# Optimization experiments

Hardware: AMD Instinct MI355X
Metric: run time of the kernel (lower is better)

The kernel has to match this reference:

```python
import jax, jax.numpy as jnp
import numpy as np

C = 128      # hidden_dim
H = 8        # nheads
HD = C // H  # head_dim = 16
SCALE = HD ** (-0.5)
Q = 100      # num_queries
T = 5        # t
DM = 512     # d_model
AD = 128     # audio feature dim
EPS = 1e-5


def _ln(x, g, b):
    m = jnp.mean(x, -1, keepdims=True)
    v = jnp.mean((x - m) ** 2, -1, keepdims=True)
    return (x - m) / jnp.sqrt(v + EPS) * g + b


def _heads(x):
    bt, L, c = x.shape
    return x.reshape(bt, L, H, c // H).transpose(0, 2, 1, 3)  # (bt,H,L,hd)


def _unheads(x):
    bt, h, L, d = x.shape
    return x.transpose(0, 2, 1, 3).reshape(bt, L, h * d)


def _attn(q, k, v):
    a = jax.nn.softmax(jnp.einsum('bhqd,bhkd->bhqk', q, k) * SCALE, axis=-1)
    return jnp.einsum('bhqk,bhkd->bhqd', a, v)


def setup_inputs() -> dict:
    key = jax.random.key(0)
    ks = iter(jax.random.split(key, 40))
    def nrm(shape, s=0.02):
        return jax.random.normal(next(ks), shape, dtype=jnp.float32) * s
    bt, hw = 40, 1024
    return {
        'audio_feat': jax.random.normal(next(ks), (bt, hw, AD), dtype=jnp.float32),
        'vis_feat': jax.random.normal(next(ks), (bt, hw, DM), dtype=jnp.float32),
        'iq_emb': nrm((Q, C), 0.1),
        'w_iqp': nrm((C, 2 * C)), 'b_iqp': jnp.zeros((2 * C,), jnp.float32),
        'w_afp': nrm((AD, 2 * C)), 'b_afp': jnp.zeros((2 * C,), jnp.float32),
        'w_vfp': nrm((DM, 2 * C)), 'b_vfp': jnp.zeros((2 * C,), jnp.float32),
        'g_an': jnp.ones((2 * C,), jnp.float32), 'be_an': jnp.zeros((2 * C,), jnp.float32),
        'g_vn': jnp.ones((2 * C,), jnp.float32), 'be_vn': jnp.zeros((2 * C,), jnp.float32),
        'w_aqp': nrm((C, 2 * C)), 'b_aqp': jnp.zeros((2 * C,), jnp.float32),
        'w_vqp': nrm((C, 2 * C)), 'b_vqp': jnp.zeros((2 * C,), jnp.float32),
        'w_aq': nrm((AD, C)), 'b_aq': jnp.zeros((C,), jnp.float32),
        'w_vq': nrm((DM, C)), 'b_vq': jnp.zeros((C,), jnp.float32),
        'w_in': nrm((C, 3 * C)), 'b_in': jnp.zeros((3 * C,), jnp.float32),
        'w_o': nrm((C, C)), 'b_o': jnp.zeros((C,), jnp.float32),
        'w_ao': nrm((C, DM)), 'b_ao': jnp.zeros((DM,), jnp.float32),
        'w_vo': nrm((C, DM)), 'b_vo': jnp.zeros((DM,), jnp.float32),
    }


def reference(audio_feat, vis_feat, iq_emb, w_iqp, b_iqp, w_afp, b_afp,
              w_vfp, b_vfp, g_an, be_an, g_vn, be_vn, w_aqp, b_aqp,
              w_vqp, b_vqp, w_aq, b_aq, w_vq, b_vq, w_in, b_in, w_o, b_o,
              w_ao, b_ao, w_vo, b_vo):
    bt, hw, _ = vis_feat.shape
    bs = bt // T

    # intermediate query projection -> audio / vis query sets
    aq0, vq0 = jnp.split(iq_emb @ w_iqp + b_iqp, 2, axis=-1)  # (Q, C) each
    aqh = _heads(jnp.broadcast_to(aq0, (bt, Q, C)))
    vqh = _heads(jnp.broadcast_to(vq0, (bt, Q, C)))

    # feature K/V (LayerNorm over 2C then chunk)
    a_ki, a_vi = jnp.split(_ln(audio_feat @ w_afp + b_afp, g_an, be_an), 2, axis=-1)
    v_ki, v_vi = jnp.split(_ln(vis_feat @ w_vfp + b_vfp, g_vn, be_vn), 2, axis=-1)

    # cross-attn: queries attend to features, with residual on queries
    aiq = _unheads(_attn(aqh, _heads(a_ki), _heads(a_vi)) + aqh)  # (bt,Q,C)
    viq = _unheads(_attn(vqh, _heads(v_ki), _heads(v_vi)) + vqh)

    # self-attn over concatenated queries across time (per sample)
    queries = jnp.concatenate([aiq, viq], axis=1).reshape(bs, T * 2 * Q, C)
    qkv = queries @ w_in + b_in
    q, k, v = jnp.split(qkv, 3, axis=-1)
    sa = _unheads(_attn(_heads(q), _heads(k), _heads(v))) @ w_o + b_o
    queries = sa.reshape(bt, 2 * Q, C)
    aiq2, viq2 = queries[:, :Q], queries[:, Q:]

    # fused queries become K/V for the features
    a_kf, a_vf = jnp.split(aiq2 @ w_aqp + b_aqp, 2, axis=-1)
    v_kf, v_vf = jnp.split(viq2 @ w_vqp + b_vqp, 2, axis=-1)
    _a = _heads(audio_feat @ w_aq + b_aq)
    _v = _heads(vis_feat @ w_vq + b_vq)

    a_att = _unheads(_attn(_a, _heads(v_kf), _heads(v_vf)))  # (bt,hw,C)
    audio_out = (a_att + audio_feat) @ w_ao + b_ao            # (bt,hw,DM)

    v_att = _unheads(_attn(_v, _heads(a_kf), _heads(a_vf)))   # (bt,hw,C)
    vis_out = v_att @ w_vo + b_vo + vis_feat                  # (bt,hw,DM)

    return (audio_out, vis_out, aiq2)
```

## Files before the change

kernel.cpp:

```cpp
#include <hip/hip_runtime.h>

#define EPSF 1e-5f
#define SCALEF 0.25f

typedef __attribute__((ext_vector_type(8))) __bf16 bf16x8;
typedef __attribute__((ext_vector_type(8))) unsigned short sh8;
typedef __attribute__((ext_vector_type(4))) float f32x4;

__device__ __forceinline__ unsigned short f2bf(float f) {
  unsigned u = __float_as_uint(f);
  return (unsigned short)((u + 0x7FFFu + ((u >> 16) & 1u)) >> 16);
}
__device__ __forceinline__ unsigned pk2(float lo, float hi) {
  return (unsigned)f2bf(lo) | ((unsigned)f2bf(hi) << 16);
}
__device__ __forceinline__ float bf2f(unsigned short u) {
  return __uint_as_float((unsigned)u << 16);
}

__device__ __forceinline__ void gll16(const void* g, void* l) {
  __builtin_amdgcn_global_load_lds((const __attribute__((address_space(1))) void*)g,
                                   (__attribute__((address_space(3))) void*)l,
                                   16, 0, 0);
}

template <int K, int BN, int EPI, bool POST, bool AHEAD, bool OBF, bool PBF>
__global__ __launch_bounds__(BN * 2) void mfma_gemm(
    const unsigned short* __restrict__ A, const unsigned short* __restrict__ Wt,
    const float* __restrict__ bias, const float* __restrict__ gg,
    const float* __restrict__ be, const float* __restrict__ post,
    float* __restrict__ C, int M, int Ntot, int ATPB, int CTPB, size_t CPS,
    float* __restrict__ aiq2) {
  constexpr int NW = BN / 32;
  constexpr int NCW = BN / 64;
  __shared__ __align__(16) unsigned short As[128 * 32];
  __shared__ __align__(16) unsigned short Bs[BN * 32];
  __shared__ float2 part[128][4];
  const int tid = threadIdx.x;
  const int wid = tid >> 6, lane = tid & 63;
  const int wr = wid / NCW, wc = wid % NCW;
  const int m0t = blockIdx.x * 128, n0t = blockIdx.y * BN;
  const int ir = lane >> 2, sl = lane & 3;
  const int sg = lane >> 4, li = lane & 15;
  f32x4 acc[4][4];
#pragma unroll
  for (int i = 0; i < 4; i++)
#pragma unroll
    for (int j = 0; j < 4; j++) acc[i][j] = (f32x4){0.f, 0.f, 0.f, 0.f};
  constexpr int nIss = 8 + BN / 16;

  for (int k0 = 0; k0 < K; k0 += 32) {
    __syncthreads();
    for (int is = wid; is < nIss; is += NW) {
      if (is < 8) {
        int r = is * 16 + ir;
        int sp = sl ^ ((r >> 1) & 3);
        const unsigned short* gsrc;
        if (AHEAD) {
          int rg = m0t + r;
          if (rg >= M) rg = M - 1;
          int b = rg / ATPB, tok = rg - b * ATPB;
          int e = k0 + sp * 8;
          gsrc = A + ((((size_t)b * 8 + (e >> 4)) * ATPB + tok) << 4) + (e & 15);
        } else {
          gsrc = A + (size_t)(m0t + r) * K + k0 + sp * 8;
        }
        gll16(gsrc, (void*)&As[is * 512]);
      } else {
        int r = (is - 8) * 16 + ir;
        int sp = sl ^ ((r >> 1) & 3);
        gll16(Wt + (size_t)(n0t + r) * K + k0 + sp * 8, (void*)&Bs[(is - 8) * 512]);
      }
    }
    __syncthreads();
    bf16x8 af[4], bfr[4];
#pragma unroll
    for (int mi = 0; mi < 4; mi++) {
      int m = wr * 64 + mi * 16 + li;
      sh8 t = *(const sh8*)&As[m * 32 + ((sg ^ ((m >> 1) & 3)) << 3)];
      af[mi] = __builtin_bit_cast(bf16x8, t);
    }
#pragma unroll
    for (int ni = 0; ni < 4; ni++) {
      int n = wc * 64 + ni * 16 + li;
      sh8 t = *(const sh8*)&Bs[n * 32 + ((sg ^ ((n >> 1) & 3)) << 3)];
      bfr[ni] = __builtin_bit_cast(bf16x8, t);
    }
#pragma unroll
    for (int mi = 0; mi < 4; mi++)
#pragma unroll
      for (int ni = 0; ni < 4; ni++)
        acc[mi][ni] = __builtin_amdgcn_mfma_f32_16x16x32_bf16(af[mi], bfr[ni],
                                                              acc[mi][ni], 0, 0, 0);
  }

  float bv[4];
#pragma unroll
  for (int ni = 0; ni < 4; ni++) bv[ni] = bias[n0t + wc * 64 + ni * 16 + li];

  if constexpr (EPI == 1) {
#pragma unroll
    for (int mi = 0; mi < 4; mi++)
#pragma unroll
      for (int ni = 0; ni < 4; ni++)
#pragma unroll
        for (int r = 0; r < 4; r++) acc[mi][ni][r] += bv[ni];
#pragma unroll
    for (int mi = 0; mi < 4; mi++)
#pragma unroll
      for (int r = 0; r < 4; r++) {
        float s = acc[mi][0][r] + acc[mi][1][r] + acc[mi][2][r] + acc[mi][3][r];
        float q2 = acc[mi][0][r] * acc[mi][0][r] + acc[mi][1][r] * acc[mi][1][r] +
                   acc[mi][2][r] * acc[mi][2][r] + acc[mi][3][r] * acc[mi][3][r];
#pragma unroll
        for (int off = 1; off < 16; off <<= 1) {
          s += __shfl_xor(s, off);
          q2 += __shfl_xor(q2, off);
        }
        if (li == 0) part[wr * 64 + mi * 16 + sg * 4 + r][wc] = make_float2(s, q2);
      }
    __syncthreads();
    float gv[4], bev[4];
#pragma unroll
    for (int ni = 0; ni < 4; ni++) {
      int col = wc * 64 + ni * 16 + li;
      gv[ni] = gg[col];
      bev[ni] = be[col];
    }
#pragma unroll
    for (int mi = 0; mi < 4; mi++)
#pragma unroll
      for (int r = 0; r < 4; r++) {
        int mrow = wr * 64 + mi * 16 + sg * 4 + r;
        float2 p0 = part[mrow][0], p1 = part[mrow][1], p2 = part[mrow][2], p3 = part[mrow][3];
        float S = p0.x + p1.x + p2.x + p3.x;
        float Qq = p0.y + p1.y + p2.y + p3.y;
        float mean = S * (1.f / 256.f);
        float var = Qq * (1.f / 256.f) - mean * mean;
        float rstd = rsqrtf(var + EPSF);
        int mg = m0t + mrow;
        int b = mg / CTPB, tok = mg - b * CTPB;
#pragma unroll
        for (int ni = 0; ni < 4; ni++) {
          int col = wc * 64 + ni * 16 + li;
          float val = (acc[mi][ni][r] - mean) * rstd * gv[ni] + bev[ni];
          int half = col >> 7, h = (col >> 4) & 7, d = col & 15;
          size_t idx = ((((size_t)b * 8 + h) * CTPB + tok) << 4) + d;
          if (OBF) {
            unsigned short* dst = (unsigned short*)C + (half ? CPS : 0);
            dst[idx] = f2bf(val);
          } else {
            float* dst = half ? (C + CPS) : C;
            dst[idx] = val;
          }
        }
      }
  } else if constexpr (EPI == 2) {
#pragma unroll
    for (int mi = 0; mi < 4; mi++)
#pragma unroll
      for (int r = 0; r < 4; r++) {
        int mg = m0t + wr * 64 + mi * 16 + sg * 4 + r;
        if (mg < M) {
          int b = mg / CTPB, tok = mg - b * CTPB;
#pragma unroll
          for (int ni = 0; ni < 4; ni++) {
            int col = n0t + wc * 64 + ni * 16 + li;
            float v = acc[mi][ni][r] + bv[ni];
            int pt = col >> 7, h = (col >> 4) & 7, d = col & 15;
            size_t idx = ((((size_t)b * 8 + h) * CTPB + tok) << 4) + d;
            if (OBF)
              ((unsigned short*)C + (size_t)pt * CPS)[idx] = f2bf(v);
            else
              (C + (size_t)pt * CPS)[idx] = v;
          }
        }
      }
  } else {
#pragma unroll
    for (int mi = 0; mi < 4; mi++)
#pragma unroll
      for (int r = 0; r < 4; r++) {
        int mrow = m0t + wr * 64 + mi * 16 + sg * 4 + r;
        if (mrow < M) {
#pragma unroll
          for (int ni = 0; ni < 4; ni++) {
            int col = n0t + wc * 64 + ni * 16 + li;
            float v = acc[mi][ni][r] + bv[ni];
            if (POST) {
              if (PBF)
                v += bf2f(((const unsigned short*)post)[(size_t)mrow * Ntot + col]);
              else
                v += post[(size_t)mrow * Ntot + col];
            }
            C[(size_t)mrow * Ntot + col] = v;
            if (aiq2) {
              int fb = mrow / 200, wi2 = mrow % 200;
              if (wi2 < 100) aiq2[((size_t)fb * 100 + wi2) * Ntot + col] = v;
            }
          }
        }
      }
  }
}

__global__ __launch_bounds__(512) void mattn1(
    const float* __restrict__ aqvq,
    const unsigned short* __restrict__ akn, const unsigned short* __restrict__ avn,
    const unsigned short* __restrict__ vkn, const unsigned short* __restrict__ vvn,
    unsigned short* __restrict__ op) {
  __shared__ __align__(16) unsigned short Klds[64][24];
  __shared__ __align__(16) unsigned short VTlds[16][72];
  __shared__ __align__(16) unsigned short Plds[8][16][72];
  const int tid = threadIdx.x, wid = tid >> 6, lane = tid & 63;
  const int li = lane & 15, gr = lane >> 4;
  const int z = blockIdx.z, h = blockIdx.y;
  const int mod = z >= 40 ? 1 : 0;
  const int b = z - mod * 40;
  const int bh = b * 8 + h;
  const int qi = wid * 16 + li;
  const bool qact = qi < 100;
  const int qic = qact ? qi : 99;
  const float* qrow = aqvq + mod * 128 + (size_t)qic * 256 + h * 16;
  const unsigned short* kp = mod ? vkn : akn;
  const unsigned short* vp = mod ? vvn : avn;

  sh8 z8 = (sh8)0;
  bf16x8 qf = __builtin_bit_cast(bf16x8, z8);
  if (gr < 2) {
    const float4* q4 = (const float4*)(qrow + gr * 8);
    float4 qa = q4[0], qb = q4[1];
    sh8 tt;
    tt[0] = f2bf(qa.x); tt[1] = f2bf(qa.y); tt[2] = f2bf(qa.z); tt[3] = f2bf(qa.w);
    tt[4] = f2bf(qb.x); tt[5] = f2bf(qb.y); tt[6] = f2bf(qb.z); tt[7] = f2bf(qb.w);
    qf = __builtin_bit_cast(bf16x8, tt);
  }

  float mrun = -3e38f, lrun = 0.f;
  f32x4 acc = (f32x4){0.f, 0.f, 0.f, 0.f};
  const f32x4 zero4 = (f32x4){0.f, 0.f, 0.f, 0.f};
  const unsigned* Ku = (const unsigned*)(kp + (size_t)bh * 1024 * 16);
  const unsigned* Vu = (const unsigned*)(vp + (size_t)bh * 1024 * 16);
  const int skey = tid >> 3, sdb = tid & 7;

  for (int kb = 0; kb < 1024; kb += 64) {
    __syncthreads();
    unsigned kw = Ku[(size_t)(kb + skey) * 8 + sdb];
    unsigned vw = Vu[(size_t)(kb + skey) * 8 + sdb];
    *(unsigned*)&Klds[skey][sdb * 2] = kw;
    VTlds[sdb * 2 + 0][skey] = (unsigned short)(kw, vw & 0xffff);
    VTlds[sdb * 2 + 1][skey] = (unsigned short)(vw >> 16);
    __syncthreads();
    f32x4 st[4];
#pragma unroll
    for (int t = 0; t < 4; t++) {
      sh8 kk = *(const sh8*)&Klds[t * 16 + li][(gr & 1) * 8];
      st[t] = __builtin_amdgcn_mfma_f32_16x16x32_bf16(
          __builtin_bit_cast(bf16x8, kk), qf, zero4, 0, 0, 0);
    }
    float sv[4][4];
#pragma unroll
    for (int t = 0; t < 4; t++)
#pragma unroll
      for (int r = 0; r < 4; r++) sv[t][r] = st[t][r] * SCALEF;
    float bm = sv[0][0];
#pragma unroll
    for (int t = 0; t < 4; t++)
#pragma unroll
      for (int r = 0; r < 4; r++) bm = fmaxf(bm, sv[t][r]);
    bm = fmaxf(bm, __shfl_xor(bm, 16));
    bm = fmaxf(bm, __shfl_xor(bm, 32));
    float mnew = fmaxf(mrun, bm);
    float cf = __expf(mrun - mnew);
    mrun = mnew;
    lrun *= cf;
    acc[0] *= cf; acc[1] *= cf; acc[2] *= cf; acc[3] *= cf;
    float ls = 0.f;
    unsigned pw[4][2];
#pragma unroll
    for (int t = 0; t < 4; t++) {
      float p0 = __expf(sv[t][0] - mnew), p1 = __expf(sv[t][1] - mnew);
      float p2 = __expf(sv[t][2] - mnew), p3 = __expf(sv[t][3] - mnew);
      ls += (p0 + p1) + (p2 + p3);
      pw[t][0] = pk2(p0, p1);
      pw[t][1] = pk2(p2, p3);
    }
    ls += __shfl_xor(ls, 16);
    ls += __shfl_xor(ls, 32);
    lrun += ls;
#pragma unroll
    for (int t = 0; t < 4; t++)
      *(uint2*)&Plds[wid][li][t * 16 + gr * 4] = make_uint2(pw[t][0], pw[t][1]);
#pragma unroll
    for (int hh = 0; hh < 2; hh++) {
      sh8 vt = *(const sh8*)&VTlds[li][hh * 32 + gr * 8];
      sh8 pt = *(const sh8*)&Plds[wid][li][hh * 32 + gr * 8];
      acc = __builtin_amdgcn_mfma_f32_16x16x32_bf16(
          __builtin_bit_cast(bf16x8, vt), __builtin_bit_cast(bf16x8, pt), acc, 0, 0, 0);
    }
  }
  float inv = 1.f / lrun;
  float o[4];
#pragma unroll
  for (int r = 0; r < 4; r++) o[r] = acc[r] * inv;
  const float4* q4 = (const float4*)(qrow + gr * 4);
  float4 qv = q4[0];
  o[0] += qv.x; o[1] += qv.y; o[2] += qv.z; o[3] += qv.w;
  if (qact) {
    int obh = (b / 5) * 8 + h;
    int otok = (b % 5) * 200 + mod * 100 + qi;
    *(uint2*)(op + (((size_t)obh * 1000 + otok) << 4) + gr * 4) =
        make_uint2(pk2(o[0], o[1]), pk2(o[2], o[3]));
  }
}

template <int MODE>
__global__ __launch_bounds__(512) void mattn8(
    const unsigned short* __restrict__ q0s, const unsigned short* __restrict__ q1s,
    size_t qsb, size_t qsh, int qsr,
    const unsigned short* __restrict__ k0s, const unsigned short* __restrict__ v0s,
    const unsigned short* __restrict__ k1s, const unsigned short* __restrict__ v1s,
    int nk, int nq, unsigned short* __restrict__ o0s, unsigned short* __restrict__ o1s,
    int OTPB, const unsigned short* __restrict__ residbf) {
  __shared__ __align__(16) unsigned short Klds[64][24];
  __shared__ __align__(16) unsigned short VTlds[16][72];
  __shared__ __align__(16) unsigned short Plds[8][16][72];
  const int tid = threadIdx.x, wid = tid >> 6, lane = tid & 63;
  const int li = lane & 15, gr = lane >> 4;
  const int z = blockIdx.z, h = blockIdx.y;
  int mod = 0, b = z;
  const unsigned short *qp = q0s, *kp = k0s, *vp = v0s;
  unsigned short* op = o0s;
  if (MODE == 2) {
    mod = z >= 40 ? 1 : 0;
    b = z - mod * 40;
    if (mod) { qp = q1s; kp = k1s; vp = v1s; op = o1s; }
  }
  const int bh = b * 8 + h;
  const int qi = blockIdx.x * 128 + wid * 16 + li;
  const bool qact = qi < nq;
  const int qic = qact ? qi : nq - 1;
  const unsigned short* qrow = qp + b * qsb + h * qsh + (size_t)qic * qsr;

  sh8 z8 = (sh8)0;
  bf16x8 qf = __builtin_bit_cast(bf16x8, z8);
  if (gr < 2) qf = __builtin_bit_cast(bf16x8, *(const sh8*)(qrow + gr * 8));

  float mrun = -3e38f, lrun = 0.f;
  f32x4 acc = (f32x4){0.f, 0.f, 0.f, 0.f};
  const f32x4 zero4 = (f32x4){0.f, 0.f, 0.f, 0.f};
  const unsigned* Ku = (const unsigned*)(kp + (size_t)bh * nk * 16);
  const unsigned* Vu = (const unsigned*)(vp + (size_t)bh * nk * 16);
  const int skey = tid >> 3, sdb = tid & 7;

  for (int kb = 0; kb < nk; kb += 64) {
    __syncthreads();
    int gk = kb + skey;
    bool ok = gk < nk;
    unsigned kw = ok ? Ku[(size_t)gk * 8 + sdb] : 0u;
    unsigned vw = ok ? Vu[(size_t)gk * 8 + sdb] : 0u;
    *(unsigned*)&Klds[skey][sdb * 2] = kw;
    VTlds[sdb * 2 + 0][skey] = (unsigned short)(vw & 0xffff);
    VTlds[sdb * 2 + 1][skey] = (unsigned short)(vw >> 16);
    __syncthreads();
    f32x4 st[4];
#pragma unroll
    for (int t = 0; t < 4; t++) {
      sh8 kk = *(const sh8*)&Klds[t * 16 + li][(gr & 1) * 8];
      st[t] = __builtin_amdgcn_mfma_f32_16x16x32_bf16(
          __builtin_bit_cast(bf16x8, kk), qf, zero4, 0, 0, 0);
    }
    float sv[4][4];
#pragma unroll
    for (int t = 0; t < 4; t++)
#pragma unroll
      for (int r = 0; r < 4; r++) sv[t][r] = st[t][r] * SCALEF;
    if (kb + 64 > nk) {
#pragma unroll
      for (int t = 0; t < 4; t++) {
        int kbase = kb + t * 16 + gr * 4;
#pragma unroll
        for (int r = 0; r < 4; r++)
          if (kbase + r >= nk) sv[t][r] = -1e30f;
      }
    }
    float bm = sv[0][0];
#pragma unroll
    for (int t = 0; t < 4; t++)
#pragma unroll
      for (int r = 0; r < 4; r++) bm = fmaxf(bm, sv[t][r]);
    bm = fmaxf(bm, __shfl_xor(bm, 16));
    bm = fmaxf(bm, __shfl_xor(bm, 32));
    float mnew = fmaxf(mrun, bm);
    float cf = __expf(mrun - mnew);
    mrun = mnew;
    lrun *= cf;
    acc[0] *= cf; acc[1] *= cf; acc[2] *= cf; acc[3] *= cf;
    float ls = 0.f;
    unsigned pw[4][2];
#pragma unroll
    for (int t = 0; t < 4; t++) {
      float p0 = __expf(sv[t][0] - mnew), p1 = __expf(sv[t][1] - mnew);
      float p2 = __expf(sv[t][2] - mnew), p3 = __expf(sv[t][3] - mnew);
      ls += (p0 + p1) + (p2 + p3);
      pw[t][0] = pk2(p0, p1);
      pw[t][1] = pk2(p2, p3);
    }
    ls += __shfl_xor(ls, 16);
    ls += __shfl_xor(ls, 32);
    lrun += ls;
#pragma unroll
    for (int t = 0; t < 4; t++)
      *(uint2*)&Plds[wid][li][t * 16 + gr * 4] = make_uint2(pw[t][0], pw[t][1]);
#pragma unroll
    for (int hh = 0; hh < 2; hh++) {
      sh8 vt = *(const sh8*)&VTlds[li][hh * 32 + gr * 8];
      sh8 pt = *(const sh8*)&Plds[wid][li][hh * 32 + gr * 8];
      acc = __builtin_amdgcn_mfma_f32_16x16x32_bf16(
          __builtin_bit_cast(bf16x8, vt), __builtin_bit_cast(bf16x8, pt), acc, 0, 0, 0);
    }
  }
  float inv = 1.f / lrun;
  float o[4];
#pragma unroll
  for (int r = 0; r < 4; r++) o[r] = acc[r] * inv;
  if (MODE == 2 && mod == 0 && residbf) {
    uint2 rv = *(const uint2*)(residbf + ((size_t)b * 1024 + qic) * 128 + h * 16 + gr * 4);
    o[0] += bf2f((unsigned short)(rv.x & 0xffff));
    o[1] += bf2f((unsigned short)(rv.x >> 16));
    o[2] += bf2f((unsigned short)(rv.y & 0xffff));
    o[3] += bf2f((unsigned short)(rv.y >> 16));
  }
  if (qact) {
    *(uint2*)(op + (((size_t)bh * OTPB + qi) << 4) + gr * 4) =
        make_uint2(pk2(o[0], o[1]), pk2(o[2], o[3]));
  }
}

__global__ __launch_bounds__(256) void prep_kernel(
    const float* __restrict__ audio, const float* __restrict__ vis,
    const float* __restrict__ iq, const float* __restrict__ w_iqp,
    const float* __restrict__ b_iqp,
    const float* __restrict__ w_afp, const float* __restrict__ w_vfp,
    const float* __restrict__ w_aq, const float* __restrict__ w_vq,
    const float* __restrict__ w_in, const float* __restrict__ w_o,
    const float* __restrict__ w_ao, const float* __restrict__ w_vo,
    unsigned short* __restrict__ WT, unsigned short* __restrict__ audio_bf,
    unsigned short* __restrict__ vis_bf, float* __restrict__ aqvq) {
  __shared__ float row[128];
  const int g = blockIdx.x, tid = threadIdx.x;
  if (g < 12800) {
    const float* in = (g < 2560) ? audio : vis;
    unsigned short* outp = (g < 2560) ? audio_bf : vis_bf;
    int i = (g < 2560 ? g : g - 2560) * 256 + tid;
    float4 a = ((const float4*)in)[i * 2];
    float4 b = ((const float4*)in)[i * 2 + 1];
    uint4 o;
    o.x = pk2(a.x, a.y);
    o.y = pk2(a.z, a.w);
    o.z = pk2(b.x, b.y);
    o.w = pk2(b.z, b.w);
    ((uint4*)outp)[i] = o;
  } else if (g < 14528) {
    int lg = g - 12800;
    int K, N;
    const float* W;
    unsigned dst;
    if (lg < 128)       { K = 128; N = 256; W = w_afp; dst = 0; }
    else if (lg < 640)  { K = 512; N = 256; W = w_vfp; dst = 32768;  lg -= 128; }
    else if (lg < 704)  { K = 128; N = 128; W = w_aq;  dst = 163840; lg -= 640; }
    else if (lg < 960)  { K = 512; N = 128; W = w_vq;  dst = 180224; lg -= 704; }
    else if (lg < 1152) { K = 128; N = 384; W = w_in;  dst = 245760; lg -= 960; }
    else if (lg < 1216) { K = 128; N = 128; W = w_o;   dst = 294912; lg -= 1152; }
    else if (lg < 1472) { K = 128; N = 512; W = w_ao;  dst = 311296; lg -= 1216; }
    else                { K = 128; N = 512; W = w_vo;  dst = 376832; lg -= 1472; }
    int idx = lg * 256 + tid;
    if (idx < K * N) {
      int k = idx / N, n = idx - k * N;
      WT[dst + (size_t)n * K + k] = f2bf(W[idx]);
    }
  } else {
    int r = g - 14528;
    if (tid < 128) row[tid] = iq[r * 128 + tid];
    __syncthreads();
    float acc = b_iqp[tid];
#pragma unroll 8
    for (int k = 0; k < 128; ++k) acc += row[k] * w_iqp[k * 256 + tid];
    aqvq[r * 256 + tid] = acc;
  }
}

template <int K, int N, int R>
__global__ __launch_bounds__(N) void gemm_kv_kernel(
    const float* __restrict__ in,
    const float* __restrict__ Wa, const float* __restrict__ ba,
    const float* __restrict__ Wv, const float* __restrict__ bvv,
    unsigned short* __restrict__ Ka, unsigned short* __restrict__ Va,
    unsigned short* __restrict__ Kv, unsigned short* __restrict__ Vv) {
  __shared__ float rows[R][K];
  const int sel = blockIdx.y;
  const float* W = sel ? Wv : Wa;
  const float* bias = sel ? bvv : ba;
  unsigned short* outK = sel ? Kv : Ka;
  unsigned short* outV = sel ? Vv : Va;
  const int rowoff = sel ? 100 : 0;
  int r0 = blockIdx.x * R;
  for (int e = threadIdx.x; e < R * K; e += N) {
    int rr = e / K, k = e - rr * K;
    size_t r = r0 + rr;
    size_t irx = (r / 100) * 200 + rowoff + (r % 100);
    rows[rr][k] = in[irx * K + k];
  }
  __syncthreads();
  int c = threadIdx.x;
  float acc[R];
  float bb = bias[c];
#pragma unroll
  for (int rr = 0; rr < R; rr++) acc[rr] = bb;
  for (int k = 0; k < K; k += 4) {
    float w0 = W[(size_t)k * N + c];
    float w1 = W[(size_t)(k + 1) * N + c];
    float w2 = W[(size_t)(k + 2) * N + c];
    float w3 = W[(size_t)(k + 3) * N + c];
#pragma unroll
    for (int rr = 0; rr < R; rr++) {
      float4 r4 = *reinterpret_cast<const float4*>(&rows[rr][k]);
      acc[rr] = fmaf(r4.x, w0, acc[rr]);
      acc[rr] = fmaf(r4.y, w1, acc[rr]);
      acc[rr] = fmaf(r4.z, w2, acc[rr]);
      acc[rr] = fmaf(r4.w, w3, acc[rr]);
    }
  }
  int half = c >> 7, h = (c >> 4) & 7, d = c & 15;
  unsigned short* dst = half ? outV : outK;
#pragma unroll
  for (int rr = 0; rr < R; rr++) {
    int r = r0 + rr;
    int b = r / 100, tok = r - b * 100;
    dst[((((size_t)b * 8 + h) * 100 + tok) << 4) + d] = f2bf(acc[rr]);
  }
}

extern "C" void kernel_launch(void* const* d_in, const int* in_sizes, int n_in,
                              void* d_out, int out_size, void* d_ws, size_t ws_size,
                              hipStream_t stream) {
  const float* audio = (const float*)d_in[0];
  const float* vis   = (const float*)d_in[1];
  const float* iq    = (const float*)d_in[2];
  const float* w_iqp = (const float*)d_in[3];
  const float* b_iqp = (const float*)d_in[4];
  const float* w_afp = (const float*)d_in[5];
  const float* b_afp = (const float*)d_in[6];
  const float* w_vfp = (const float*)d_in[7];
  const float* b_vfp = (const float*)d_in[8];
  const float* g_an  = (const float*)d_in[9];
  const float* be_an = (const float*)d_in[10];
  const float* g_vn  = (const float*)d_in[11];
  const float* be_vn = (const float*)d_in[12];
  const float* w_aqp = (const float*)d_in[13];
  const float* b_aqp = (const float*)d_in[14];
  const float* w_vqp = (const float*)d_in[15];
  const float* b_vqp = (const float*)d_in[16];
  const float* w_aq  = (const float*)d_in[17];
  const float* b_aq  = (const float*)d_in[18];
  const float* w_vq  = (const float*)d_in[19];
  const float* b_vq  = (const float*)d_in[20];
  const float* w_in  = (const float*)d_in[21];
  const float* b_in  = (const float*)d_in[22];
  const float* w_o   = (const float*)d_in[23];
  const float* b_o   = (const float*)d_in[24];
  const float* w_ao  = (const float*)d_in[25];
  const float* b_ao  = (const float*)d_in[26];
  const float* w_vo  = (const float*)d_in[27];
  const float* b_vo  = (const float*)d_in[28];

  float* out = (float*)d_out;
  float* ws  = (float*)d_ws;

  unsigned short* vis_bf = (unsigned short*)(out);
  unsigned short* akn = (unsigned short*)(out + 10485760);
  unsigned short* avn = akn + 5242880;
  unsigned short* vkn = akn + 10485760;
  unsigned short* vvn = akn + 15728640;
  unsigned short* a_hm = (unsigned short*)(out + 20971520);
  unsigned short* v_hm = (unsigned short*)(out + 23592960);
  float* aiq2_out = out + 41943040;
  float* audio_out = out;
  float* vis_out   = out + 20971520;

  unsigned short* WT       = (unsigned short*)(ws);
  unsigned short* audio_bf = (unsigned short*)(ws + 262144);
  unsigned short* Q1hm     = (unsigned short*)(ws + 2883584);
  unsigned short* saphm    = (unsigned short*)(ws + 3395584);
  unsigned short* qkvhm    = (unsigned short*)(ws + 3915776);
  unsigned short* aatthm   = (unsigned short*)(ws + 3915776);
  unsigned short* vatthm   = (unsigned short*)(ws + 6987776);
  float* SA                = ws + 9609216;
  unsigned short* Ka = (unsigned short*)(ws + 10633216);
  unsigned short* Va = Ka + 512000;
  unsigned short* Kv = Ka + 1024000;
  unsigned short* Vv = Ka + 1536000;
  float* aqvq = ws + 12681216;

  unsigned short* ao_t = WT + 311296;
  unsigned short* vo_t = WT + 376832;
  unsigned short* afp_t = WT + 0;
  unsigned short* vfp_t = WT + 32768;
  unsigned short* aq_t  = WT + 163840;
  unsigned short* vq_t  = WT + 180224;
  unsigned short* in_t  = WT + 245760;
  unsigned short* o_t   = WT + 294912;

  prep_kernel<<<14628, 256, 0, stream>>>(
      audio, vis, iq, w_iqp, b_iqp, w_afp, w_vfp, w_aq, w_vq, w_in, w_o, w_ao,
      w_vo, WT, audio_bf, vis_bf, aqvq);

  mfma_gemm<128, 256, 1, false, false, true, false><<<dim3(320, 1), 512, 0, stream>>>(
      audio_bf, afp_t, b_afp, g_an, be_an, nullptr, (float*)akn, 40960, 256, 0, 1024,
      5242880, nullptr);
  mfma_gemm<512, 256, 1, false, false, true, false><<<dim3(320, 1), 512, 0, stream>>>(
      vis_bf, vfp_t, b_vfp, g_vn, be_vn, nullptr, (float*)vkn, 40960, 256, 0, 1024,
      5242880, nullptr);

  mattn1<<<dim3(1, 8, 80), 512, 0, stream>>>(aqvq, akn, avn, vkn, vvn, Q1hm);

  mfma_gemm<128, 128, 2, false, true, true, false><<<dim3(63, 3), 256, 0, stream>>>(
      Q1hm, in_t, b_in, nullptr, nullptr, nullptr, (float*)qkvhm, 8000, 384, 1000, 1000,
      1024000, nullptr);

  mattn8<1><<<dim3(8, 8, 8), 512, 0, stream>>>(
      qkvhm, nullptr, 128000, 16000, 16, qkvhm + 1024000, qkvhm + 2048000,
      nullptr, nullptr, 1000, 1000, saphm, nullptr, 1000, nullptr);

  mfma_gemm<128, 128, 0, false, true, false, false><<<dim3(63, 1), 256, 0, stream>>>(
      saphm, o_t, b_o, nullptr, nullptr, nullptr, SA, 8000, 128, 1000, 0, 0, aiq2_out);

  gemm_kv_kernel<128, 256, 16><<<dim3(250, 2), 256, 0, stream>>>(
      SA, w_aqp, b_aqp, w_vqp, b_vqp, Ka, Va, Kv, Vv);

  mfma_gemm<128, 128, 2, false, false, true, false><<<dim3(320, 1), 256, 0, stream>>>(
      audio_bf, aq_t, b_aq, nullptr, nullptr, nullptr, (float*)a_hm, 40960, 128, 0, 1024,
      0, nullptr);
  mfma_gemm<512, 128, 2, false, false, true, false><<<dim3(320, 1), 256, 0, stream>>>(
      vis_bf, vq_t, b_vq, nullptr, nullptr, nullptr, (float*)v_hm, 40960, 128, 0, 1024,
      0, nullptr);

  mattn8<2><<<dim3(8, 8, 80), 512, 0, stream>>>(
      a_hm, v_hm, 131072, 16384, 16, Kv, Vv, Ka, Va, 100, 1024,
      aatthm, vatthm, 1024, audio_bf);

  mfma_gemm<128, 128, 0, true, true, false, true><<<dim3(320, 4), 256, 0, stream>>>(
      vatthm, vo_t, b_vo, nullptr, nullptr, (const float*)vis_bf, vis_out, 40960, 512,
      1024, 0, 0, nullptr);

  mfma_gemm<128, 128, 0, false, true, false, false><<<dim3(320, 4), 256, 0, stream>>>(
      aatthm, ao_t, b_ao, nullptr, nullptr, nullptr, audio_out, 40960, 512, 1024, 0, 0,
      nullptr);
}
```

Before: 348.4 us.

## Fuse fp32-to-bf16 input conversion into first projection GEMMs and prefetch attention K/V

The standalone pass that converted audio and visual features to bf16 is removed. The first projection GEMMs now read fp32 directly, convert to bf16 in registers, and store the tile into LDS and into a side bf16 buffer that later kernels reuse. The attention kernels also register-prefetch the next K/V block before the barrier so the global loads overlap compute. In exchange, the A loads in those GEMMs no longer go through async global-to-LDS and are issued synchronously by threads. Each converted chunk is written only once because the output dimension fits in one block column.

```diff
diff --git a/kernel.cpp b/kernel.cpp
--- a/kernel.cpp
+++ b/kernel.cpp
@@ -24,13 +24,14 @@
                                    16, 0, 0);
 }
 
-template <int K, int BN, int EPI, bool POST, bool AHEAD, bool OBF, bool PBF>
+template <int K, int BN, int EPI, bool POST, bool AHEAD, bool OBF, bool PBF, bool AF32>
 __global__ __launch_bounds__(BN * 2) void mfma_gemm(
     const unsigned short* __restrict__ A, const unsigned short* __restrict__ Wt,
     const float* __restrict__ bias, const float* __restrict__ gg,
     const float* __restrict__ be, const float* __restrict__ post,
     float* __restrict__ C, int M, int Ntot, int ATPB, int CTPB, size_t CPS,
-    float* __restrict__ aiq2) {
+    float* __restrict__ aiq2, const float* __restrict__ Af32,
+    unsigned short* __restrict__ Aside) {
   constexpr int NW = BN / 32;
   constexpr int NCW = BN / 64;
   __shared__ __align__(16) unsigned short As[128 * 32];
@@ -51,25 +52,42 @@
 
   for (int k0 = 0; k0 < K; k0 += 32) {
     __syncthreads();
-    for (int is = wid; is < nIss; is += NW) {
-      if (is < 8) {
-        int r = is * 16 + ir;
-        int sp = sl ^ ((r >> 1) & 3);
-        const unsigned short* gsrc;
-        if (AHEAD) {
-          int rg = m0t + r;
-          if (rg >= M) rg = M - 1;
-          int b = rg / ATPB, tok = rg - b * ATPB;
-          int e = k0 + sp * 8;
-          gsrc = A + ((((size_t)b * 8 + (e >> 4)) * ATPB + tok) << 4) + (e & 15);
+    if constexpr (AF32) {
+      int r = tid >> 2, slp = tid & 3;
+      int sp = slp ^ ((r >> 1) & 3);
+      const float4* src = (const float4*)(Af32 + (size_t)(m0t + r) * K + k0 + sp * 8);
+      float4 aa = src[0], bb = src[1];
+      uint4 w;
+      w.x = pk2(aa.x, aa.y); w.y = pk2(aa.z, aa.w);
+      w.z = pk2(bb.x, bb.y); w.w = pk2(bb.z, bb.w);
+      *(uint4*)&As[r * 32 + slp * 8] = w;
+      *(uint4*)(Aside + (size_t)(m0t + r) * K + k0 + sp * 8) = w;
+      for (int is = 8 + wid; is < nIss; is += NW) {
+        int r2 = (is - 8) * 16 + ir;
+        int sp2 = sl ^ ((r2 >> 1) & 3);
+        gll16(Wt + (size_t)(n0t + r2) * K + k0 + sp2 * 8, (void*)&Bs[(is - 8) * 512]);
+      }
+    } else {
+      for (int is = wid; is < nIss; is += NW) {
+        if (is < 8) {
+          int r = is * 16 + ir;
+          int sp = sl ^ ((r >> 1) & 3);
+          const unsigned short* gsrc;
+          if (AHEAD) {
+            int rg = m0t + r;
+            if (rg >= M) rg = M - 1;
+            int b = rg / ATPB, tok = rg - b * ATPB;
+            int e = k0 + sp * 8;
+            gsrc = A + ((((size_t)b * 8 + (e >> 4)) * ATPB + tok) << 4) + (e & 15);
+          } else {
+            gsrc = A + (size_t)(m0t + r) * K + k0 + sp * 8;
+          }
+          gll16(gsrc, (void*)&As[is * 512]);
         } else {
-          gsrc = A + (size_t)(m0t + r) * K + k0 + sp * 8;
+          int r = (is - 8) * 16 + ir;
+          int sp = sl ^ ((r >> 1) & 3);
+          gll16(Wt + (size_t)(n0t + r) * K + k0 + sp * 8, (void*)&Bs[(is - 8) * 512]);
         }
-        gll16(gsrc, (void*)&As[is * 512]);
-      } else {
-        int r = (is - 8) * 16 + ir;
-        int sp = sl ^ ((r >> 1) & 3);
-        gll16(Wt + (size_t)(n0t + r) * K + k0 + sp * 8, (void*)&Bs[(is - 8) * 512]);
       }
     }
     __syncthreads();
@@ -243,13 +261,17 @@
   const unsigned* Vu = (const unsigned*)(vp + (size_t)bh * 1024 * 16);
   const int skey = tid >> 3, sdb = tid & 7;
 
+  unsigned kw = Ku[(size_t)skey * 8 + sdb];
+  unsigned vw = Vu[(size_t)skey * 8 + sdb];
   for (int kb = 0; kb < 1024; kb += 64) {
     __syncthreads();
-    unsigned kw = Ku[(size_t)(kb + skey) * 8 + sdb];
-    unsigned vw = Vu[(size_t)(kb + skey) * 8 + sdb];
     *(unsigned*)&Klds[skey][sdb * 2] = kw;
-    VTlds[sdb * 2 + 0][skey] = (unsigned short)(kw, vw & 0xffff);
+    VTlds[sdb * 2 + 0][skey] = (unsigned short)(vw & 0xffff);
     VTlds[sdb * 2 + 1][skey] = (unsigned short)(vw >> 16);
+    if (kb + 64 < 1024) {
+      kw = Ku[(size_t)(kb + 64 + skey) * 8 + sdb];
+      vw = Vu[(size_t)(kb + 64 + skey) * 8 + sdb];
+    }
     __syncthreads();
     f32x4 st[4];
 #pragma unroll
@@ -353,15 +375,18 @@
   const unsigned* Vu = (const unsigned*)(vp + (size_t)bh * nk * 16);
   const int skey = tid >> 3, sdb = tid & 7;
 
+  unsigned kw = (skey < nk) ? Ku[(size_t)skey * 8 + sdb] : 0u;
+  unsigned vw = (skey < nk) ? Vu[(size_t)skey * 8 + sdb] : 0u;
   for (int kb = 0; kb < nk; kb += 64) {
     __syncthreads();
-    int gk = kb + skey;
-    bool ok = gk < nk;
-    unsigned kw = ok ? Ku[(size_t)gk * 8 + sdb] : 0u;
-    unsigned vw = ok ? Vu[(size_t)gk * 8 + sdb] : 0u;
     *(unsigned*)&Klds[skey][sdb * 2] = kw;
     VTlds[sdb * 2 + 0][skey] = (unsigned short)(vw & 0xffff);
     VTlds[sdb * 2 + 1][skey] = (unsigned short)(vw >> 16);
+    if (kb + 64 < nk) {
+      int gk = kb + 64 + skey;
+      kw = (gk < nk) ? Ku[(size_t)gk * 8 + sdb] : 0u;
+      vw = (gk < nk) ? Vu[(size_t)gk * 8 + sdb] : 0u;
+    }
     __syncthreads();
     f32x4 st[4];
 #pragma unroll
@@ -438,31 +463,17 @@
 }
 
 __global__ __launch_bounds__(256) void prep_kernel(
-    const float* __restrict__ audio, const float* __restrict__ vis,
     const float* __restrict__ iq, const float* __restrict__ w_iqp,
     const float* __restrict__ b_iqp,
     const float* __restrict__ w_afp, const float* __restrict__ w_vfp,
     const float* __restrict__ w_aq, const float* __restrict__ w_vq,
     const float* __restrict__ w_in, const float* __restrict__ w_o,
     const float* __restrict__ w_ao, const float* __restrict__ w_vo,
-    unsigned short* __restrict__ WT, unsigned short* __restrict__ audio_bf,
-    unsigned short* __restrict__ vis_bf, float* __restrict__ aqvq) {
+    unsigned short* __restrict__ WT, float* __restrict__ aqvq) {
   __shared__ float row[128];
   const int g = blockIdx.x, tid = threadIdx.x;
-  if (g < 12800) {
-    const float* in = (g < 2560) ? audio : vis;
-    unsigned short* outp = (g < 2560) ? audio_bf : vis_bf;
-    int i = (g < 2560 ? g : g - 2560) * 256 + tid;
-    float4 a = ((const float4*)in)[i * 2];
-    float4 b = ((const float4*)in)[i * 2 + 1];
-    uint4 o;
-    o.x = pk2(a.x, a.y);
-    o.y = pk2(a.z, a.w);
-    o.z = pk2(b.x, b.y);
-    o.w = pk2(b.z, b.w);
-    ((uint4*)outp)[i] = o;
-  } else if (g < 14528) {
-    int lg = g - 12800;
+  if (g < 1728) {
+    int lg = g;
     int K, N;
     const float* W;
     unsigned dst;
@@ -480,7 +491,7 @@
       WT[dst + (size_t)n * K + k] = f2bf(W[idx]);
     }
   } else {
-    int r = g - 14528;
+    int r = g - 1728;
     if (tid < 128) row[tid] = iq[r * 128 + tid];
     __syncthreads();
     float acc = b_iqp[tid];
@@ -602,58 +613,58 @@
   unsigned short* Vv = Ka + 1536000;
   float* aqvq = ws + 12681216;
 
-  unsigned short* ao_t = WT + 311296;
-  unsigned short* vo_t = WT + 376832;
   unsigned short* afp_t = WT + 0;
   unsigned short* vfp_t = WT + 32768;
   unsigned short* aq_t  = WT + 163840;
   unsigned short* vq_t  = WT + 180224;
   unsigned short* in_t  = WT + 245760;
   unsigned short* o_t   = WT + 294912;
-
-  prep_kernel<<<14628, 256, 0, stream>>>(
-      audio, vis, iq, w_iqp, b_iqp, w_afp, w_vfp, w_aq, w_vq, w_in, w_o, w_ao,
-      w_vo, WT, audio_bf, vis_bf, aqvq);
-
-  mfma_gemm<128, 256, 1, false, false, true, false><<<dim3(320, 1), 512, 0, stream>>>(
-      audio_bf, afp_t, b_afp, g_an, be_an, nullptr, (float*)akn, 40960, 256, 0, 1024,
-      5242880, nullptr);
-  mfma_gemm<512, 256, 1, false, false, true, false><<<dim3(320, 1), 512, 0, stream>>>(
-      vis_bf, vfp_t, b_vfp, g_vn, be_vn, nullptr, (float*)vkn, 40960, 256, 0, 1024,
-      5242880, nullptr);
+  unsigned short* ao_t  = WT + 311296;
+  unsigned short* vo_t  = WT + 376832;
+
+  prep_kernel<<<1828, 256, 0, stream>>>(
+      iq, w_iqp, b_iqp, w_afp, w_vfp, w_aq, w_vq, w_in, w_o, w_ao, w_vo, WT, aqvq);
+
+  mfma_gemm<128, 256, 1, false, false, true, false, true><<<dim3(320, 1), 512, 0, stream>>>(
+      nullptr, afp_t, b_afp, g_an, be_an, nullptr, (float*)akn, 40960, 256, 0, 1024,
+      5242880, nullptr, audio, audio_bf);
+  mfma_gemm<512, 256, 1, false, false, true, false, true><<<dim3(320, 1), 512, 0, stream>>>(
+      nullptr, vfp_t, b_vfp, g_vn, be_vn, nullptr, (float*)vkn, 40960, 256, 0, 1024,
+      5242880, nullptr, vis, vis_bf);
 
   mattn1<<<dim3(1, 8, 80), 512, 0, stream>>>(aqvq, akn, avn, vkn, vvn, Q1hm);
 
-  mfma_gemm<128, 128, 2, false, true, true, false><<<dim3(63, 3), 256, 0, stream>>>(
+  mfma_gemm<128, 128, 2, false, true, true, false, false><<<dim3(63, 3), 256, 0, stream>>>(
       Q1hm, in_t, b_in, nullptr, nullptr, nullptr, (float*)qkvhm, 8000, 384, 1000, 1000,
-      1024000, nullptr);
+      1024000, nullptr, nullptr, nullptr);
 
   mattn8<1><<<dim3(8, 8, 8), 512, 0, stream>>>(
       qkvhm, nullptr, 128000, 16000, 16, qkvhm + 1024000, qkvhm + 2048000,
       nullptr, nullptr, 1000, 1000, saphm, nullptr, 1000, nullptr);
 
-  mfma_gemm<128, 128, 0, false, true, false, false><<<dim3(63, 1), 256, 0, stream>>>(
-      saphm, o_t, b_o, nullptr, nullptr, nullptr, SA, 8000, 128, 1000, 0, 0, aiq2_out);
+  mfma_gemm<128, 128, 0, false, true, false, false, false><<<dim3(63, 1), 256, 0, stream>>>(
+      saphm, o_t, b_o, nullptr, nullptr, nullptr, SA, 8000, 128, 1000, 0, 0, aiq2_out,
+      nullptr, nullptr);
 
   gemm_kv_kernel<128, 256, 16><<<dim3(250, 2), 256, 0, stream>>>(
       SA, w_aqp, b_aqp, w_vqp, b_vqp, Ka, Va, Kv, Vv);
 
-  mfma_gemm<128, 128, 2, false, false, true, false><<<dim3(320, 1), 256, 0, stream>>>(
+  mfma_gemm<128, 128, 2, false, false, true, false, false><<<dim3(320, 1), 256, 0, stream>>>(
       audio_bf, aq_t, b_aq, nullptr, nullptr, nullptr, (float*)a_hm, 40960, 128, 0, 1024,
-      0, nullptr);
-  mfma_gemm<512, 128, 2, false, false, true, false><<<dim3(320, 1), 256, 0, stream>>>(
+      0, nullptr, nullptr, nullptr);
+  mfma_gemm<512, 128, 2, false, false, true, false, false><<<dim3(320, 1), 256, 0, stream>>>(
       vis_bf, vq_t, b_vq, nullptr, nullptr, nullptr, (float*)v_hm, 40960, 128, 0, 1024,
-      0, nullptr);
+      0, nullptr, nullptr, nullptr);
 
   mattn8<2><<<dim3(8, 8, 80), 512, 0, stream>>>(
       a_hm, v_hm, 131072, 16384, 16, Kv, Vv, Ka, Va, 100, 1024,
       aatthm, vatthm, 1024, audio_bf);
 
-  mfma_gemm<128, 128, 0, true, true, false, true><<<dim3(320, 4), 256, 0, stream>>>(
+  mfma_gemm<128, 128, 0, true, true, false, true, false><<<dim3(320, 4), 256, 0, stream>>>(
       vatthm, vo_t, b_vo, nullptr, nullptr, (const float*)vis_bf, vis_out, 40960, 512,
-      1024, 0, 0, nullptr);
-
-  mfma_gemm<128, 128, 0, false, true, false, false><<<dim3(320, 4), 256, 0, stream>>>(
+      1024, 0, 0, nullptr, nullptr, nullptr);
+
+  mfma_gemm<128, 128, 0, false, true, false, false, false><<<dim3(320, 4), 256, 0, stream>>>(
       aatthm, ao_t, b_ao, nullptr, nullptr, nullptr, audio_out, 40960, 512, 1024, 0, 0,
-      nullptr);
-}
+      nullptr, nullptr, nullptr);
+}
```

New measurement: 339.5 us. 1.03x faster.
